# Kernel optimization log

Hardware: AMD Instinct MI355X
Metric: run time of the kernel (lower is better)

## Reference

```python
import jax, jax.numpy as jnp
import numpy as np

N_NODES = 200000  # num_users + num_items
N_EDGES = 1000000
D = 64


def setup_inputs() -> dict:
    key = jax.random.key(0)
    ks = jax.random.split(key, 9)
    return {
        "src": jax.random.randint(ks[0], (N_EDGES,), 0, N_NODES, dtype=jnp.int32),
        "dst": jax.random.randint(ks[1], (N_EDGES,), 0, N_NODES, dtype=jnp.int32),
        "review_feat": jax.random.normal(ks[2], (N_EDGES, D), dtype=jnp.float32),
        "ci_r": jax.random.uniform(ks[3], (N_NODES, 1), dtype=jnp.float32),
        "feature": jax.random.normal(ks[4], (N_NODES, D), dtype=jnp.float32),
        "W1": jax.random.normal(ks[5], (D, D), dtype=jnp.float32) * 0.05,
        "W2": jax.random.normal(ks[6], (D, D), dtype=jnp.float32) * 0.05,
        "feature2": jax.random.normal(ks[7], (N_NODES, D), dtype=jnp.float32) * 0.05,
        "feature3": jax.random.normal(ks[8], (N_NODES, D), dtype=jnp.float32) * 0.05,
    }


def reference(src, dst, review_feat, ci_r, feature, W1, W2, feature2, feature3):
    # Eval-mode forward (is_training=False, freeze='', dropout = identity).
    # `feature` is assigned to g.srcdata['h_r'] in the original but never used.
    n = ci_r.shape[0]
    ci_src = ci_r[src]            # [E,1] gather of src norm coeff
    ci_dst = ci_r                 # [N,1]

    # Pass 1: edge linear on review features, scaled by src coeff, scatter-sum.
    r = review_feat @ W1.T                                   # [E,64]
    h1 = jax.ops.segment_sum(r * ci_src, dst, num_segments=n)
    rst_re = h1 * ci_dst

    # Pass 2: (src embedding + edge transform) messages.
    r_fe = review_feat @ W2.T                                # [E,64]
    m2 = (feature2[src] + r_fe) * ci_src
    h2 = jax.ops.segment_sum(m2, dst, num_segments=n)
    rst = h2 * ci_dst

    # Pass 3: pure src-embedding messages.
    m3 = feature3[src] * ci_src
    h3 = jax.ops.segment_sum(m3, dst, num_segments=n)
    rst_id = h3 * ci_dst

    return (rst, rst_re, rst_id)
```

## Files before the change

### kernel.cpp

```cpp
#include <hip/hip_runtime.h>

#define NN 200000
#define NE 1000000
#define DD 64
#define NCHUNK 196

typedef __bf16 bf16x4 __attribute__((ext_vector_type(4)));
typedef __bf16 bf16x8 __attribute__((ext_vector_type(8)));
typedef float  f32x4  __attribute__((ext_vector_type(4)));

static __device__ __forceinline__ bf16x8 pack8(const float* __restrict__ p) {
    float4 a = *reinterpret_cast<const float4*>(p);
    float4 b = *reinterpret_cast<const float4*>(p + 4);
    bf16x8 r;
    r[0] = (__bf16)a.x; r[1] = (__bf16)a.y; r[2] = (__bf16)a.z; r[3] = (__bf16)a.w;
    r[4] = (__bf16)b.x; r[5] = (__bf16)b.y; r[6] = (__bf16)b.z; r[7] = (__bf16)b.w;
    return r;
}

static __device__ __forceinline__ bf16x8 pack8s(const float* __restrict__ p, float c) {
    float4 a = *reinterpret_cast<const float4*>(p);
    float4 b = *reinterpret_cast<const float4*>(p + 4);
    bf16x8 r;
    r[0] = (__bf16)(a.x * c); r[1] = (__bf16)(a.y * c);
    r[2] = (__bf16)(a.z * c); r[3] = (__bf16)(a.w * c);
    r[4] = (__bf16)(b.x * c); r[5] = (__bf16)(b.y * c);
    r[6] = (__bf16)(b.z * c); r[7] = (__bf16)(b.w * c);
    return r;
}

__global__ __launch_bounds__(256) void k_prep(
    const int* __restrict__ dst, const float* __restrict__ f2,
    const float* __restrict__ f3, const float* __restrict__ ci,
    int* __restrict__ counts, __bf16* __restrict__ f2c, __bf16* __restrict__ f3c)
{
    const int b = blockIdx.x;
    if (b < 1024) {
        for (int e = b * 256 + threadIdx.x; e < NE; e += 1024 * 256)
            atomicAdd(&counts[dst[e]], 1);
    } else {
        const size_t per = (size_t)NN * DD / 8;
        const size_t stride = (size_t)(gridDim.x - 1024) * 256;
        for (size_t i = (size_t)(b - 1024) * 256 + threadIdx.x; i < per; i += stride) {
            const int row = (int)(i >> 3);
            const float c = ci[row];
            *reinterpret_cast<bf16x8*>(f2c + i * 8) = pack8s(f2 + i * 8, c);
            *reinterpret_cast<bf16x8*>(f3c + i * 8) = pack8s(f3 + i * 8, c);
        }
    }
}

__global__ __launch_bounds__(256) void k_chunk_sums(const int* __restrict__ counts,
                                                    int* __restrict__ csum) {
    const int b = blockIdx.x, tid = threadIdx.x;
    const int base = b * 1024 + tid * 4;
    int s = 0;
#pragma unroll
    for (int j = 0; j < 4; ++j) {
        const int i = base + j;
        if (i < NN) s += counts[i];
    }
#pragma unroll
    for (int d = 32; d > 0; d >>= 1) s += __shfl_down(s, d);
    __shared__ int wsum[4];
    if ((tid & 63) == 0) wsum[tid >> 6] = s;
    __syncthreads();
    if (tid == 0) csum[b] = wsum[0] + wsum[1] + wsum[2] + wsum[3];
}

__global__ void k_scan_chunks(const int* __restrict__ csum, int* __restrict__ cofs) {
    if (threadIdx.x == 0 && blockIdx.x == 0) {
        int acc = 0;
        for (int i = 0; i < NCHUNK; ++i) { cofs[i] = acc; acc += csum[i]; }
    }
}

__global__ __launch_bounds__(256) void k_chunk_scan(const int* __restrict__ counts,
                                                    const int* __restrict__ cofs,
                                                    int* __restrict__ offs,
                                                    int* __restrict__ cursor) {
    const int b = blockIdx.x, tid = threadIdx.x;
    const int lane = tid & 63, wv = tid >> 6;
    const int base = b * 1024 + tid * 4;
    int c[4];
#pragma unroll
    for (int j = 0; j < 4; ++j) {
        const int i = base + j;
        c[j] = (i < NN) ? counts[i] : 0;
    }
    const int ls = c[0] + c[1] + c[2] + c[3];
    int v = ls;
#pragma unroll
    for (int d = 1; d < 64; d <<= 1) {
        const int u = __shfl_up(v, d);
        if (lane >= d) v += u;
    }
    __shared__ int wsum[4];
    if (lane == 63) wsum[wv] = v;
    __syncthreads();
    int wbase = 0;
    for (int w = 0; w < wv; ++w) wbase += wsum[w];
    int excl = cofs[b] + wbase + (v - ls);
#pragma unroll
    for (int j = 0; j < 4; ++j) {
        const int i = base + j;
        if (i < NN) { offs[i] = excl; cursor[i] = excl; }
        excl += c[j];
    }
}

__global__ __launch_bounds__(256) void k_permfill(const int* __restrict__ dst,
                                                  const int* __restrict__ src,
                                                  const float* __restrict__ ci,
                                                  int* __restrict__ cursor,
                                                  int4* __restrict__ epack) {
    for (int e = blockIdx.x * blockDim.x + threadIdx.x; e < NE;
         e += gridDim.x * blockDim.x) {
        const int s = src[e];
        const float cs = ci[s];
        const int pos = atomicAdd(&cursor[dst[e]], 1);
        epack[pos] = make_int4(e, s, __float_as_int(cs), 0);
    }
}

__global__ __launch_bounds__(256) void k_pull_fused(
    const int4* __restrict__ epack, const int* __restrict__ offs,
    const int* __restrict__ counts, const float* __restrict__ review,
    const float* __restrict__ ci,
    const __bf16* __restrict__ f2c, const __bf16* __restrict__ f3c,
    const float* __restrict__ W1, const float* __restrict__ W2,
    float* __restrict__ out_rst, float* __restrict__ out_re,
    float* __restrict__ out_id)
{
    __shared__ __bf16 At[16][64];
    __shared__ float  S2[16][64];

    const int tid = threadIdx.x;
    const int l16 = tid & 15;
    const int q   = tid >> 4;
    const int n   = blockIdx.x * 16 + q;

    const int beg = offs[n];
    const int cnt = counts[n];

    float4 ax0 = {0,0,0,0}, a20 = {0,0,0,0}, a30 = {0,0,0,0};
    float4 ax1 = {0,0,0,0}, a21 = {0,0,0,0}, a31 = {0,0,0,0};

    int k = 0;
    for (; k + 2 <= cnt; k += 2) {
        const int4 ea = epack[beg + k];
        const int4 eb = epack[beg + k + 1];
        const float ca = __int_as_float(ea.z);
        const float cb = __int_as_float(eb.z);
        const float4 ra = *reinterpret_cast<const float4*>(review + (size_t)ea.x * DD + l16 * 4);
        const float4 rb = *reinterpret_cast<const float4*>(review + (size_t)eb.x * DD + l16 * 4);
        const bf16x4 p2a = *reinterpret_cast<const bf16x4*>(f2c + (size_t)ea.y * DD + l16 * 4);
        const bf16x4 p2b = *reinterpret_cast<const bf16x4*>(f2c + (size_t)eb.y * DD + l16 * 4);
        const bf16x4 p3a = *reinterpret_cast<const bf16x4*>(f3c + (size_t)ea.y * DD + l16 * 4);
        const bf16x4 p3b = *reinterpret_cast<const bf16x4*>(f3c + (size_t)eb.y * DD + l16 * 4);
        ax0.x = fmaf(ra.x, ca, ax0.x); ax0.y = fmaf(ra.y, ca, ax0.y);
        ax0.z = fmaf(ra.z, ca, ax0.z); ax0.w = fmaf(ra.w, ca, ax0.w);
        ax1.x = fmaf(rb.x, cb, ax1.x); ax1.y = fmaf(rb.y, cb, ax1.y);
        ax1.z = fmaf(rb.z, cb, ax1.z); ax1.w = fmaf(rb.w, cb, ax1.w);
        a20.x += (float)p2a[0]; a20.y += (float)p2a[1];
        a20.z += (float)p2a[2]; a20.w += (float)p2a[3];
        a21.x += (float)p2b[0]; a21.y += (float)p2b[1];
        a21.z += (float)p2b[2]; a21.w += (float)p2b[3];
        a30.x += (float)p3a[0]; a30.y += (float)p3a[1];
        a30.z += (float)p3a[2]; a30.w += (float)p3a[3];
        a31.x += (float)p3b[0]; a31.y += (float)p3b[1];
        a31.z += (float)p3b[2]; a31.w += (float)p3b[3];
    }
    if (k < cnt) {
        const int4 ea = epack[beg + k];
        const float ca = __int_as_float(ea.z);
        const float4 ra = *reinterpret_cast<const float4*>(review + (size_t)ea.x * DD + l16 * 4);
        const bf16x4 p2a = *reinterpret_cast<const bf16x4*>(f2c + (size_t)ea.y * DD + l16 * 4);
        const bf16x4 p3a = *reinterpret_cast<const bf16x4*>(f3c + (size_t)ea.y * DD + l16 * 4);
        ax0.x = fmaf(ra.x, ca, ax0.x); ax0.y = fmaf(ra.y, ca, ax0.y);
        ax0.z = fmaf(ra.z, ca, ax0.z); ax0.w = fmaf(ra.w, ca, ax0.w);
        a20.x += (float)p2a[0]; a20.y += (float)p2a[1];
        a20.z += (float)p2a[2]; a20.w += (float)p2a[3];
        a30.x += (float)p3a[0]; a30.y += (float)p3a[1];
        a30.z += (float)p3a[2]; a30.w += (float)p3a[3];
    }

    const float cid = ci[n];
    float4 ax = {ax0.x + ax1.x, ax0.y + ax1.y, ax0.z + ax1.z, ax0.w + ax1.w};
    float4 a2 = {a20.x + a21.x, a20.y + a21.y, a20.z + a21.z, a20.w + a21.w};
    float4 a3 = {a30.x + a31.x, a30.y + a31.y, a30.z + a31.z, a30.w + a31.w};

    float4 v3 = {a3.x * cid, a3.y * cid, a3.z * cid, a3.w * cid};
    *reinterpret_cast<float4*>(out_id + (size_t)n * DD + l16 * 4) = v3;

    bf16x4 hb;
    hb[0] = (__bf16)(ax.x * cid); hb[1] = (__bf16)(ax.y * cid);
    hb[2] = (__bf16)(ax.z * cid); hb[3] = (__bf16)(ax.w * cid);
    *reinterpret_cast<bf16x4*>(&At[q][l16 * 4]) = hb;
    float4 s2v = {a2.x * cid, a2.y * cid, a2.z * cid, a2.w * cid};
    *reinterpret_cast<float4*>(&S2[q][l16 * 4]) = s2v;
    __syncthreads();

    const int w  = tid >> 6;
    const int lq = (tid & 63) >> 4;
    bf16x8 w1f[2], w2f[2];
#pragma unroll
    for (int kk = 0; kk < 2; ++kk) {
        const int off = (w * 16 + l16) * DD + kk * 32 + lq * 8;
        w1f[kk] = pack8(W1 + off);
        w2f[kk] = pack8(W2 + off);
    }
    const bf16x8 a0 = *reinterpret_cast<const bf16x8*>(&At[l16][lq * 8]);
    const bf16x8 a1 = *reinterpret_cast<const bf16x8*>(&At[l16][lq * 8 + 32]);

    const f32x4 zero = {0.f, 0.f, 0.f, 0.f};
    f32x4 acc1 = zero, acc2 = zero;
    acc1 = __builtin_amdgcn_mfma_f32_16x16x32_bf16(a0, w1f[0], acc1, 0, 0, 0);
    acc1 = __builtin_amdgcn_mfma_f32_16x16x32_bf16(a1, w1f[1], acc1, 0, 0, 0);
    acc2 = __builtin_amdgcn_mfma_f32_16x16x32_bf16(a0, w2f[0], acc2, 0, 0, 0);
    acc2 = __builtin_amdgcn_mfma_f32_16x16x32_bf16(a1, w2f[1], acc2, 0, 0, 0);

    const int base = blockIdx.x * 16;
#pragma unroll
    for (int i = 0; i < 4; ++i) {
        const int row = lq * 4 + i;
        const size_t o = (size_t)(base + row) * DD + w * 16 + l16;
        out_re[o]  = acc1[i];
        out_rst[o] = acc2[i] + S2[row][w * 16 + l16];
    }
}

__global__ __launch_bounds__(256) void gcn_mfma_kernel(
    const int* __restrict__ src, const int* __restrict__ dst,
    const float* __restrict__ review, const float* __restrict__ ci,
    const float* __restrict__ W1, const float* __restrict__ W2,
    const float* __restrict__ f2, const float* __restrict__ f3,
    float* __restrict__ out)
{
    float* out_rst = out;
    float* out_re  = out + (size_t)NN * DD;
    float* out_id  = out + 2 * (size_t)NN * DD;
    const int lane = threadIdx.x & 63;
    const int l16  = lane & 15;
    const int lq   = lane >> 4;
    const int wid  = blockIdx.x * (blockDim.x >> 6) + (threadIdx.x >> 6);
    const int nw   = gridDim.x * (blockDim.x >> 6);

    bf16x8 w1f[4][2], w2f[4][2];
#pragma unroll
    for (int c = 0; c < 4; ++c)
#pragma unroll
        for (int kk = 0; kk < 2; ++kk) {
            const int off = (c * 16 + l16) * DD + kk * 32 + lq * 8;
            w1f[c][kk] = pack8(W1 + off);
            w2f[c][kk] = pack8(W2 + off);
        }
    const f32x4 zero = {0.f, 0.f, 0.f, 0.f};
    for (int t = wid; t < NE / 16; t += nw) {
        const int e0 = t * 16;
        const float* xr = review + (size_t)(e0 + l16) * DD + lq * 8;
        const bf16x8 a0 = pack8(xr);
        const bf16x8 a1 = pack8(xr + 32);
        f32x4 acc1[4], acc2[4];
#pragma unroll
        for (int c = 0; c < 4; ++c) { acc1[c] = zero; acc2[c] = zero; }
#pragma unroll
        for (int c = 0; c < 4; ++c) {
            acc1[c] = __builtin_amdgcn_mfma_f32_16x16x32_bf16(a0, w1f[c][0], acc1[c], 0, 0, 0);
            acc1[c] = __builtin_amdgcn_mfma_f32_16x16x32_bf16(a1, w1f[c][1], acc1[c], 0, 0, 0);
            acc2[c] = __builtin_amdgcn_mfma_f32_16x16x32_bf16(a0, w2f[c][0], acc2[c], 0, 0, 0);
            acc2[c] = __builtin_amdgcn_mfma_f32_16x16x32_bf16(a1, w2f[c][1], acc2[c], 0, 0, 0);
        }
        int sA[4], dA[4]; float cf[4];
#pragma unroll
        for (int i = 0; i < 4; ++i) {
            const int e = e0 + lq * 4 + i;
            sA[i] = src[e]; dA[i] = dst[e];
            cf[i] = ci[sA[i]] * ci[dA[i]];
        }
#pragma unroll
        for (int i = 0; i < 4; ++i) {
            const size_t so = (size_t)sA[i] * DD;
            const size_t dofs = (size_t)dA[i] * DD;
            const float c_ = cf[i];
#pragma unroll
            for (int c = 0; c < 4; ++c) {
                const int col = c * 16 + l16;
                atomicAdd(out_re  + dofs + col, acc1[c][i] * c_);
                atomicAdd(out_rst + dofs + col, (f2[so + col] + acc2[c][i]) * c_);
                atomicAdd(out_id  + dofs + col, f3[so + col] * c_);
            }
        }
    }
}

extern "C" void kernel_launch(void* const* d_in, const int* in_sizes, int n_in,
                              void* d_out, int out_size, void* d_ws, size_t ws_size,
                              hipStream_t stream) {
    const int*   src    = (const int*)d_in[0];
    const int*   dst    = (const int*)d_in[1];
    const float* review = (const float*)d_in[2];
    const float* ci     = (const float*)d_in[3];
    const float* W1     = (const float*)d_in[5];
    const float* W2     = (const float*)d_in[6];
    const float* f2     = (const float*)d_in[7];
    const float* f3     = (const float*)d_in[8];
    float* out = (float*)d_out;
    float* out_rst = out;
    float* out_re  = out + (size_t)NN * DD;
    float* out_id  = out + 2 * (size_t)NN * DD;

    const size_t NEED = sizeof(int) * ((size_t)3 * NN + 512) +
                        sizeof(int4) * (size_t)NE +
                        2 * sizeof(__bf16) * (size_t)NN * DD;
    if (ws_size < NEED) {
        hipMemsetAsync(out, 0, (size_t)out_size * sizeof(float), stream);
        gcn_mfma_kernel<<<2048, 256, 0, stream>>>(src, dst, review, ci, W1, W2, f2, f3, out);
        return;
    }

    char* w = (char*)d_ws;
    int* counts = (int*)w;    w += (size_t)NN * 4;
    int* offs   = (int*)w;    w += (size_t)NN * 4;
    int* cursor = (int*)w;    w += (size_t)NN * 4;
    int* csum   = (int*)w;    w += 256 * 4;
    int* cofs   = (int*)w;    w += 256 * 4;
    int4* epack = (int4*)w;   w += (size_t)NE * 16;
    __bf16* f2c = (__bf16*)w; w += (size_t)NN * DD * 2;
    __bf16* f3c = (__bf16*)w;

    hipMemsetAsync(counts, 0, (size_t)NN * 4, stream);
    k_prep      <<<3072, 256, 0, stream>>>(dst, f2, f3, ci, counts, f2c, f3c);
    k_chunk_sums<<<NCHUNK, 256, 0, stream>>>(counts, csum);
    k_scan_chunks<<<1, 64, 0, stream>>>(csum, cofs);
    k_chunk_scan<<<NCHUNK, 256, 0, stream>>>(counts, cofs, offs, cursor);
    k_permfill  <<<1024, 256, 0, stream>>>(dst, src, ci, cursor, epack);
    k_pull_fused<<<NN / 16, 256, 0, stream>>>(epack, offs, counts, review, ci,
                                              f2c, f3c, W1, W2,
                                              out_rst, out_re, out_id);
}
```

Baseline: 294.7 us.

## Pre-scale review rows into dst-sorted bf16 messages during permutation fill

The permutation-fill kernel now reads each review row sequentially, scales it by the source coefficient, converts it to bf16 and writes it at its dst-sorted slot, along with a compact src index array. The pull kernel then streams these messages contiguously instead of gathering fp32 review rows by edge id. This trades random fp32 gathers for a coalesced read plus scattered bf16 writes and an extra 128MB intermediate buffer. Rounding the messages to bf16 adds precision loss in the review path.

```diff
diff --git a/kernel.cpp b/kernel.cpp
--- a/kernel.cpp
+++ b/kernel.cpp
@@ -109,23 +109,32 @@
     }
 }
 
-__global__ __launch_bounds__(256) void k_permfill(const int* __restrict__ dst,
-                                                  const int* __restrict__ src,
-                                                  const float* __restrict__ ci,
-                                                  int* __restrict__ cursor,
-                                                  int4* __restrict__ epack) {
-    for (int e = blockIdx.x * blockDim.x + threadIdx.x; e < NE;
-         e += gridDim.x * blockDim.x) {
-        const int s = src[e];
-        const float cs = ci[s];
-        const int pos = atomicAdd(&cursor[dst[e]], 1);
-        epack[pos] = make_int4(e, s, __float_as_int(cs), 0);
-    }
+__global__ __launch_bounds__(256) void k_permfill_msg(
+    const int* __restrict__ dst, const int* __restrict__ src,
+    const float* __restrict__ ci, const float* __restrict__ review,
+    int* __restrict__ cursor, __bf16* __restrict__ mrev, int* __restrict__ srcs)
+{
+    const int tid = threadIdx.x;
+    const int l16 = tid & 15;
+    const int e   = blockIdx.x * 16 + (tid >> 4);
+
+    const int s = src[e];
+    const float cs = ci[s];
+    int pos = 0;
+    if (l16 == 0) pos = atomicAdd(&cursor[dst[e]], 1);
+    pos = __shfl(pos, tid & 48);
+
+    const float4 r = *reinterpret_cast<const float4*>(review + (size_t)e * DD + l16 * 4);
+    bf16x4 m;
+    m[0] = (__bf16)(r.x * cs); m[1] = (__bf16)(r.y * cs);
+    m[2] = (__bf16)(r.z * cs); m[3] = (__bf16)(r.w * cs);
+    *reinterpret_cast<bf16x4*>(mrev + (size_t)pos * DD + l16 * 4) = m;
+    if (l16 == 0) srcs[pos] = s;
 }
 
 __global__ __launch_bounds__(256) void k_pull_fused(
-    const int4* __restrict__ epack, const int* __restrict__ offs,
-    const int* __restrict__ counts, const float* __restrict__ review,
+    const __bf16* __restrict__ mrev, const int* __restrict__ srcs,
+    const int* __restrict__ offs, const int* __restrict__ counts,
     const float* __restrict__ ci,
     const __bf16* __restrict__ f2c, const __bf16* __restrict__ f3c,
     const float* __restrict__ W1, const float* __restrict__ W2,
@@ -148,20 +157,18 @@
 
     int k = 0;
     for (; k + 2 <= cnt; k += 2) {
-        const int4 ea = epack[beg + k];
-        const int4 eb = epack[beg + k + 1];
-        const float ca = __int_as_float(ea.z);
-        const float cb = __int_as_float(eb.z);
-        const float4 ra = *reinterpret_cast<const float4*>(review + (size_t)ea.x * DD + l16 * 4);
-        const float4 rb = *reinterpret_cast<const float4*>(review + (size_t)eb.x * DD + l16 * 4);
-        const bf16x4 p2a = *reinterpret_cast<const bf16x4*>(f2c + (size_t)ea.y * DD + l16 * 4);
-        const bf16x4 p2b = *reinterpret_cast<const bf16x4*>(f2c + (size_t)eb.y * DD + l16 * 4);
-        const bf16x4 p3a = *reinterpret_cast<const bf16x4*>(f3c + (size_t)ea.y * DD + l16 * 4);
-        const bf16x4 p3b = *reinterpret_cast<const bf16x4*>(f3c + (size_t)eb.y * DD + l16 * 4);
-        ax0.x = fmaf(ra.x, ca, ax0.x); ax0.y = fmaf(ra.y, ca, ax0.y);
-        ax0.z = fmaf(ra.z, ca, ax0.z); ax0.w = fmaf(ra.w, ca, ax0.w);
-        ax1.x = fmaf(rb.x, cb, ax1.x); ax1.y = fmaf(rb.y, cb, ax1.y);
-        ax1.z = fmaf(rb.z, cb, ax1.z); ax1.w = fmaf(rb.w, cb, ax1.w);
+        const int sa = srcs[beg + k];
+        const int sb = srcs[beg + k + 1];
+        const bf16x4 ma = *reinterpret_cast<const bf16x4*>(mrev + (size_t)(beg + k) * DD + l16 * 4);
+        const bf16x4 mb = *reinterpret_cast<const bf16x4*>(mrev + (size_t)(beg + k + 1) * DD + l16 * 4);
+        const bf16x4 p2a = *reinterpret_cast<const bf16x4*>(f2c + (size_t)sa * DD + l16 * 4);
+        const bf16x4 p2b = *reinterpret_cast<const bf16x4*>(f2c + (size_t)sb * DD + l16 * 4);
+        const bf16x4 p3a = *reinterpret_cast<const bf16x4*>(f3c + (size_t)sa * DD + l16 * 4);
+        const bf16x4 p3b = *reinterpret_cast<const bf16x4*>(f3c + (size_t)sb * DD + l16 * 4);
+        ax0.x += (float)ma[0]; ax0.y += (float)ma[1];
+        ax0.z += (float)ma[2]; ax0.w += (float)ma[3];
+        ax1.x += (float)mb[0]; ax1.y += (float)mb[1];
+        ax1.z += (float)mb[2]; ax1.w += (float)mb[3];
         a20.x += (float)p2a[0]; a20.y += (float)p2a[1];
         a20.z += (float)p2a[2]; a20.w += (float)p2a[3];
         a21.x += (float)p2b[0]; a21.y += (float)p2b[1];
@@ -172,13 +179,12 @@
         a31.z += (float)p3b[2]; a31.w += (float)p3b[3];
     }
     if (k < cnt) {
-        const int4 ea = epack[beg + k];
-        const float ca = __int_as_float(ea.z);
-        const float4 ra = *reinterpret_cast<const float4*>(review + (size_t)ea.x * DD + l16 * 4);
-        const bf16x4 p2a = *reinterpret_cast<const bf16x4*>(f2c + (size_t)ea.y * DD + l16 * 4);
-        const bf16x4 p3a = *reinterpret_cast<const bf16x4*>(f3c + (size_t)ea.y * DD + l16 * 4);
-        ax0.x = fmaf(ra.x, ca, ax0.x); ax0.y = fmaf(ra.y, ca, ax0.y);
-        ax0.z = fmaf(ra.z, ca, ax0.z); ax0.w = fmaf(ra.w, ca, ax0.w);
+        const int sa = srcs[beg + k];
+        const bf16x4 ma = *reinterpret_cast<const bf16x4*>(mrev + (size_t)(beg + k) * DD + l16 * 4);
+        const bf16x4 p2a = *reinterpret_cast<const bf16x4*>(f2c + (size_t)sa * DD + l16 * 4);
+        const bf16x4 p3a = *reinterpret_cast<const bf16x4*>(f3c + (size_t)sa * DD + l16 * 4);
+        ax0.x += (float)ma[0]; ax0.y += (float)ma[1];
+        ax0.z += (float)ma[2]; ax0.w += (float)ma[3];
         a20.x += (float)p2a[0]; a20.y += (float)p2a[1];
         a20.z += (float)p2a[2]; a20.w += (float)p2a[3];
         a30.x += (float)p3a[0]; a30.y += (float)p3a[1];
@@ -310,9 +316,9 @@
     float* out_re  = out + (size_t)NN * DD;
     float* out_id  = out + 2 * (size_t)NN * DD;
 
-    const size_t NEED = sizeof(int) * ((size_t)3 * NN + 512) +
-                        sizeof(int4) * (size_t)NE +
-                        2 * sizeof(__bf16) * (size_t)NN * DD;
+    const size_t NEED = sizeof(int) * ((size_t)3 * NN + 512 + NE) +
+                        2 * sizeof(__bf16) * (size_t)NN * DD +
+                        sizeof(__bf16) * (size_t)NE * DD;
     if (ws_size < NEED) {
         hipMemsetAsync(out, 0, (size_t)out_size * sizeof(float), stream);
         gcn_mfma_kernel<<<2048, 256, 0, stream>>>(src, dst, review, ci, W1, W2, f2, f3, out);
@@ -325,17 +331,18 @@
     int* cursor = (int*)w;    w += (size_t)NN * 4;
     int* csum   = (int*)w;    w += 256 * 4;
     int* cofs   = (int*)w;    w += 256 * 4;
-    int4* epack = (int4*)w;   w += (size_t)NE * 16;
+    int* srcs   = (int*)w;    w += (size_t)NE * 4;
     __bf16* f2c = (__bf16*)w; w += (size_t)NN * DD * 2;
-    __bf16* f3c = (__bf16*)w;
+    __bf16* f3c = (__bf16*)w; w += (size_t)NN * DD * 2;
+    __bf16* mrev = (__bf16*)w;
 
     hipMemsetAsync(counts, 0, (size_t)NN * 4, stream);
-    k_prep      <<<3072, 256, 0, stream>>>(dst, f2, f3, ci, counts, f2c, f3c);
-    k_chunk_sums<<<NCHUNK, 256, 0, stream>>>(counts, csum);
-    k_scan_chunks<<<1, 64, 0, stream>>>(csum, cofs);
-    k_chunk_scan<<<NCHUNK, 256, 0, stream>>>(counts, cofs, offs, cursor);
-    k_permfill  <<<1024, 256, 0, stream>>>(dst, src, ci, cursor, epack);
-    k_pull_fused<<<NN / 16, 256, 0, stream>>>(epack, offs, counts, review, ci,
-                                              f2c, f3c, W1, W2,
-                                              out_rst, out_re, out_id);
-}
+    k_prep        <<<3072, 256, 0, stream>>>(dst, f2, f3, ci, counts, f2c, f3c);
+    k_chunk_sums  <<<NCHUNK, 256, 0, stream>>>(counts, csum);
+    k_scan_chunks <<<1, 64, 0, stream>>>(csum, cofs);
+    k_chunk_scan  <<<NCHUNK, 256, 0, stream>>>(counts, cofs, offs, cursor);
+    k_permfill_msg<<<NE / 16, 256, 0, stream>>>(dst, src, ci, review, cursor, mrev, srcs);
+    k_pull_fused  <<<NN / 16, 256, 0, stream>>>(mrev, srcs, offs, counts, ci,
+                                                f2c, f3c, W1, W2,
+                                                out_rst, out_re, out_id);
+}
```

New measurement: 318.3 us. 1.08x slower.

## Split fused pull+GEMM into separate gather and MFMA GEMM kernels

Applied to the files above, without the earlier changes.

Un-fuses the pull kernel. The gather now writes the aggregated review sum in bf16 to a workspace buffer and writes the f2 part directly to out_rst. A new GEMM kernel does 16 rows by 64 columns per wave, with W1/W2 held in registers, and adds its result to out_rst. This removes the shared-memory sync and the per-block W reloads from the latency-bound gather, at the cost of an extra bf16 round trip and a read-modify-write of out_rst. It also replaces the memset with a zero kernel and adds nontemporal stores.

```diff
diff --git a/kernel.cpp b/kernel.cpp
--- a/kernel.cpp
+++ b/kernel.cpp
@@ -27,6 +27,12 @@
     r[4] = (__bf16)(b.x * c); r[5] = (__bf16)(b.y * c);
     r[6] = (__bf16)(b.z * c); r[7] = (__bf16)(b.w * c);
     return r;
+}
+
+__global__ __launch_bounds__(256) void k_zero(int* __restrict__ counts) {
+    const int i = (blockIdx.x * 256 + threadIdx.x) * 4;
+    if (i + 3 < NN) *reinterpret_cast<int4*>(counts + i) = make_int4(0, 0, 0, 0);
+    else for (int j = i; j < NN; ++j) counts[j] = 0;
 }
 
 __global__ __launch_bounds__(256) void k_prep(
@@ -123,22 +129,17 @@
     }
 }
 
-__global__ __launch_bounds__(256) void k_pull_fused(
+__global__ __launch_bounds__(256) void k_pull(
     const int4* __restrict__ epack, const int* __restrict__ offs,
     const int* __restrict__ counts, const float* __restrict__ review,
     const float* __restrict__ ci,
     const __bf16* __restrict__ f2c, const __bf16* __restrict__ f3c,
-    const float* __restrict__ W1, const float* __restrict__ W2,
-    float* __restrict__ out_rst, float* __restrict__ out_re,
+    __bf16* __restrict__ hxb, float* __restrict__ out_rst,
     float* __restrict__ out_id)
 {
-    __shared__ __bf16 At[16][64];
-    __shared__ float  S2[16][64];
-
     const int tid = threadIdx.x;
     const int l16 = tid & 15;
-    const int q   = tid >> 4;
-    const int n   = blockIdx.x * 16 + q;
+    const int n   = blockIdx.x * 16 + (tid >> 4);
 
     const int beg = offs[n];
     const int cnt = counts[n];
@@ -152,8 +153,8 @@
         const int4 eb = epack[beg + k + 1];
         const float ca = __int_as_float(ea.z);
         const float cb = __int_as_float(eb.z);
-        const float4 ra = *reinterpret_cast<const float4*>(review + (size_t)ea.x * DD + l16 * 4);
-        const float4 rb = *reinterpret_cast<const float4*>(review + (size_t)eb.x * DD + l16 * 4);
+        const float4 ra  = *reinterpret_cast<const float4*>(review + (size_t)ea.x * DD + l16 * 4);
+        const float4 rb  = *reinterpret_cast<const float4*>(review + (size_t)eb.x * DD + l16 * 4);
         const bf16x4 p2a = *reinterpret_cast<const bf16x4*>(f2c + (size_t)ea.y * DD + l16 * 4);
         const bf16x4 p2b = *reinterpret_cast<const bf16x4*>(f2c + (size_t)eb.y * DD + l16 * 4);
         const bf16x4 p3a = *reinterpret_cast<const bf16x4*>(f3c + (size_t)ea.y * DD + l16 * 4);
@@ -174,7 +175,7 @@
     if (k < cnt) {
         const int4 ea = epack[beg + k];
         const float ca = __int_as_float(ea.z);
-        const float4 ra = *reinterpret_cast<const float4*>(review + (size_t)ea.x * DD + l16 * 4);
+        const float4 ra  = *reinterpret_cast<const float4*>(review + (size_t)ea.x * DD + l16 * 4);
         const bf16x4 p2a = *reinterpret_cast<const bf16x4*>(f2c + (size_t)ea.y * DD + l16 * 4);
         const bf16x4 p3a = *reinterpret_cast<const bf16x4*>(f3c + (size_t)ea.y * DD + l16 * 4);
         ax0.x = fmaf(ra.x, ca, ax0.x); ax0.y = fmaf(ra.y, ca, ax0.y);
@@ -186,47 +187,69 @@
     }
 
     const float cid = ci[n];
-    float4 ax = {ax0.x + ax1.x, ax0.y + ax1.y, ax0.z + ax1.z, ax0.w + ax1.w};
-    float4 a2 = {a20.x + a21.x, a20.y + a21.y, a20.z + a21.z, a20.w + a21.w};
-    float4 a3 = {a30.x + a31.x, a30.y + a31.y, a30.z + a31.z, a30.w + a31.w};
-
-    float4 v3 = {a3.x * cid, a3.y * cid, a3.z * cid, a3.w * cid};
-    *reinterpret_cast<float4*>(out_id + (size_t)n * DD + l16 * 4) = v3;
+    const float4 ax = {ax0.x + ax1.x, ax0.y + ax1.y, ax0.z + ax1.z, ax0.w + ax1.w};
+    const float4 a2 = {a20.x + a21.x, a20.y + a21.y, a20.z + a21.z, a20.w + a21.w};
+    const float4 a3 = {a30.x + a31.x, a30.y + a31.y, a30.z + a31.z, a30.w + a31.w};
+
+    f32x4 v3 = {a3.x * cid, a3.y * cid, a3.z * cid, a3.w * cid};
+    __builtin_nontemporal_store(v3, reinterpret_cast<f32x4*>(out_id + (size_t)n * DD + l16 * 4));
+
+    f32x4 v2 = {a2.x * cid, a2.y * cid, a2.z * cid, a2.w * cid};
+    *reinterpret_cast<f32x4*>(out_rst + (size_t)n * DD + l16 * 4) = v2;
 
     bf16x4 hb;
     hb[0] = (__bf16)(ax.x * cid); hb[1] = (__bf16)(ax.y * cid);
     hb[2] = (__bf16)(ax.z * cid); hb[3] = (__bf16)(ax.w * cid);
-    *reinterpret_cast<bf16x4*>(&At[q][l16 * 4]) = hb;
-    float4 s2v = {a2.x * cid, a2.y * cid, a2.z * cid, a2.w * cid};
-    *reinterpret_cast<float4*>(&S2[q][l16 * 4]) = s2v;
-    __syncthreads();
-
-    const int w  = tid >> 6;
-    const int lq = (tid & 63) >> 4;
-    bf16x8 w1f[2], w2f[2];
-#pragma unroll
-    for (int kk = 0; kk < 2; ++kk) {
-        const int off = (w * 16 + l16) * DD + kk * 32 + lq * 8;
-        w1f[kk] = pack8(W1 + off);
-        w2f[kk] = pack8(W2 + off);
-    }
-    const bf16x8 a0 = *reinterpret_cast<const bf16x8*>(&At[l16][lq * 8]);
-    const bf16x8 a1 = *reinterpret_cast<const bf16x8*>(&At[l16][lq * 8 + 32]);
+    *reinterpret_cast<bf16x4*>(hxb + (size_t)n * DD + l16 * 4) = hb;
+}
+
+__global__ __launch_bounds__(256) void k_gemm(
+    const __bf16* __restrict__ hxb, const float* __restrict__ W1,
+    const float* __restrict__ W2, float* __restrict__ out_re,
+    float* __restrict__ out_rst)
+{
+    const int lane = threadIdx.x & 63;
+    const int l16  = lane & 15;
+    const int lq   = lane >> 4;
+    const int t = blockIdx.x * (blockDim.x >> 6) + (threadIdx.x >> 6);
+    if (t >= NN / 16) return;
+
+    bf16x8 w1f[4][2], w2f[4][2];
+#pragma unroll
+    for (int c = 0; c < 4; ++c)
+#pragma unroll
+        for (int kk = 0; kk < 2; ++kk) {
+            const int off = (c * 16 + l16) * DD + kk * 32 + lq * 8;
+            w1f[c][kk] = pack8(W1 + off);
+            w2f[c][kk] = pack8(W2 + off);
+        }
+
+    const int n0 = t * 16;
+    const __bf16* xr = hxb + (size_t)(n0 + l16) * DD + lq * 8;
+    const bf16x8 a0 = *reinterpret_cast<const bf16x8*>(xr);
+    const bf16x8 a1 = *reinterpret_cast<const bf16x8*>(xr + 32);
 
     const f32x4 zero = {0.f, 0.f, 0.f, 0.f};
-    f32x4 acc1 = zero, acc2 = zero;
-    acc1 = __builtin_amdgcn_mfma_f32_16x16x32_bf16(a0, w1f[0], acc1, 0, 0, 0);
-    acc1 = __builtin_amdgcn_mfma_f32_16x16x32_bf16(a1, w1f[1], acc1, 0, 0, 0);
-    acc2 = __builtin_amdgcn_mfma_f32_16x16x32_bf16(a0, w2f[0], acc2, 0, 0, 0);
-    acc2 = __builtin_amdgcn_mfma_f32_16x16x32_bf16(a1, w2f[1], acc2, 0, 0, 0);
-
-    const int base = blockIdx.x * 16;
+    f32x4 acc1[4], acc2[4];
+#pragma unroll
+    for (int c = 0; c < 4; ++c) { acc1[c] = zero; acc2[c] = zero; }
+#pragma unroll
+    for (int c = 0; c < 4; ++c) {
+        acc1[c] = __builtin_amdgcn_mfma_f32_16x16x32_bf16(a0, w1f[c][0], acc1[c], 0, 0, 0);
+        acc1[c] = __builtin_amdgcn_mfma_f32_16x16x32_bf16(a1, w1f[c][1], acc1[c], 0, 0, 0);
+        acc2[c] = __builtin_amdgcn_mfma_f32_16x16x32_bf16(a0, w2f[c][0], acc2[c], 0, 0, 0);
+        acc2[c] = __builtin_amdgcn_mfma_f32_16x16x32_bf16(a1, w2f[c][1], acc2[c], 0, 0, 0);
+    }
+
 #pragma unroll
     for (int i = 0; i < 4; ++i) {
-        const int row = lq * 4 + i;
-        const size_t o = (size_t)(base + row) * DD + w * 16 + l16;
-        out_re[o]  = acc1[i];
-        out_rst[o] = acc2[i] + S2[row][w * 16 + l16];
+        const size_t n = (size_t)(n0 + lq * 4 + i) * DD;
+#pragma unroll
+        for (int c = 0; c < 4; ++c) {
+            const int col = c * 16 + l16;
+            __builtin_nontemporal_store(acc1[c][i], out_re + n + col);
+            out_rst[n + col] += acc2[c][i];
+        }
     }
 }
 
@@ -312,9 +335,9 @@
 
     const size_t NEED = sizeof(int) * ((size_t)3 * NN + 512) +
                         sizeof(int4) * (size_t)NE +
-                        2 * sizeof(__bf16) * (size_t)NN * DD;
+                        3 * sizeof(__bf16) * (size_t)NN * DD;
     if (ws_size < NEED) {
-        hipMemsetAsync(out, 0, (size_t)out_size * sizeof(float), stream);
+        (void)hipMemsetAsync(out, 0, (size_t)out_size * sizeof(float), stream);
         gcn_mfma_kernel<<<2048, 256, 0, stream>>>(src, dst, review, ci, W1, W2, f2, f3, out);
         return;
     }
@@ -327,15 +350,16 @@
     int* cofs   = (int*)w;    w += 256 * 4;
     int4* epack = (int4*)w;   w += (size_t)NE * 16;
     __bf16* f2c = (__bf16*)w; w += (size_t)NN * DD * 2;
-    __bf16* f3c = (__bf16*)w;
-
-    hipMemsetAsync(counts, 0, (size_t)NN * 4, stream);
-    k_prep      <<<3072, 256, 0, stream>>>(dst, f2, f3, ci, counts, f2c, f3c);
-    k_chunk_sums<<<NCHUNK, 256, 0, stream>>>(counts, csum);
-    k_scan_chunks<<<1, 64, 0, stream>>>(csum, cofs);
-    k_chunk_scan<<<NCHUNK, 256, 0, stream>>>(counts, cofs, offs, cursor);
-    k_permfill  <<<1024, 256, 0, stream>>>(dst, src, ci, cursor, epack);
-    k_pull_fused<<<NN / 16, 256, 0, stream>>>(epack, offs, counts, review, ci,
-                                              f2c, f3c, W1, W2,
-                                              out_rst, out_re, out_id);
-}
+    __bf16* f3c = (__bf16*)w; w += (size_t)NN * DD * 2;
+    __bf16* hxb = (__bf16*)w;
+
+    k_zero        <<<(NN / 4 + 255) / 256, 256, 0, stream>>>(counts);
+    k_prep        <<<3072, 256, 0, stream>>>(dst, f2, f3, ci, counts, f2c, f3c);
+    k_chunk_sums  <<<NCHUNK, 256, 0, stream>>>(counts, csum);
+    k_scan_chunks <<<1, 64, 0, stream>>>(csum, cofs);
+    k_chunk_scan  <<<NCHUNK, 256, 0, stream>>>(counts, cofs, offs, cursor);
+    k_permfill    <<<1024, 256, 0, stream>>>(dst, src, ci, cursor, epack);
+    k_pull        <<<NN / 16, 256, 0, stream>>>(epack, offs, counts, review, ci,
+                                                f2c, f3c, hxb, out_rst, out_id);
+    k_gemm        <<<(NN / 16 + 3) / 4, 256, 0, stream>>>(hxb, W1, W2, out_re, out_rst);
+}
```

New measurement: 302.7 us. 2.7% more time.
